# Kernel optimization log

Measured on AMD Instinct MI355X. Metric: run time of the kernel, lower is better.

## Reference

```python
import jax, jax.numpy as jnp
import numpy as np

B, N, E, IN, H, D = 4, 50000, 800000, 128, 4, 32
GAT_SLOPE = 0.2   # DGL GATConv leaky_relu negative_slope
ACT_SLOPE = 0.01  # nn.LeakyReLU default
BN_EPS = 1e-5


def _leaky(x, slope):
    return jnp.where(x >= 0, x, slope * x)


def setup_inputs() -> dict:
    key = jax.random.key(0)
    ks = jax.random.split(key, 6)
    xx = jax.random.normal(ks[0], (B, N, IN), dtype=jnp.float32)
    W = jax.random.normal(ks[1], (IN, H * D), dtype=jnp.float32) / np.sqrt(IN).astype(np.float32)
    attn_l = jax.random.normal(ks[2], (H, D), dtype=jnp.float32) * 0.1
    attn_r = jax.random.normal(ks[3], (H, D), dtype=jnp.float32) * 0.1
    gamma = jnp.ones((H * D,), dtype=jnp.float32)
    beta = jnp.zeros((H * D,), dtype=jnp.float32)
    src = jax.random.randint(ks[4], (E,), 0, N, dtype=jnp.int32)
    dst = jax.random.randint(ks[5], (E,), 0, N, dtype=jnp.int32)
    return {"xx": xx, "W": W, "attn_l": attn_l, "attn_r": attn_r,
            "gamma": gamma, "beta": beta, "src": src, "dst": dst}


def reference(xx, W, attn_l, attn_r, gamma, beta, src, dst):
    def gat_single(x):  # x: [N, IN]
        feat = (x @ W).reshape(N, H, D)                       # [N,H,D]
        el = jnp.einsum('nhd,hd->nh', feat, attn_l)           # [N,H]
        er = jnp.einsum('nhd,hd->nh', feat, attn_r)           # [N,H]
        e = _leaky(el[src] + er[dst], GAT_SLOPE)              # [E,H]
        # edge softmax over incoming edges of each dst node (stable)
        m = jax.ops.segment_max(e, dst, num_segments=N)       # [N,H]
        m = jnp.where(jnp.isfinite(m), m, 0.0)                # zero-in-degree guard
        w = jnp.exp(e - m[dst])                               # [E,H]
        denom = jax.ops.segment_sum(w, dst, num_segments=N)   # [N,H]
        alpha = w / jnp.maximum(denom[dst], 1e-9)             # [E,H]
        # scatter-weighted aggregation
        msg = alpha[:, :, None] * feat[src]                   # [E,H,D]
        return jax.ops.segment_sum(msg, dst, num_segments=N)  # [N,H,D]

    out = jax.vmap(gat_single)(xx)                            # [B,N,H,D]
    h = out.reshape(B, N, H * D)                              # flatten(2)
    # BatchNorm1d over channel dim (stats over B and N), training-mode batch stats
    mean = h.mean(axis=(0, 1))
    var = h.var(axis=(0, 1))
    hn = (h - mean) * jax.lax.rsqrt(var + BN_EPS) * gamma + beta
    return _leaky(hn, ACT_SLOPE)                              # [B,N,H*D]
```

## Files before the change

### kernel.cpp

```cpp
#include <hip/hip_runtime.h>
#include <math.h>

#define B_ 4
#define N_ 50000
#define E_ 800000
#define IN_ 128
#define H_ 4
#define D_ 32
#define HD_ 128
#define M_ (B_*N_)
#define GR_ 32

constexpr float GAT_SLOPE = 0.2f;
constexpr float ACT_SLOPE = 0.01f;
constexpr float BN_EPS = 1e-5f;

__device__ __forceinline__ unsigned short f2bf(float x) {
    unsigned u = __float_as_uint(x);
    unsigned r = (u + 0x7FFFu + ((u >> 16) & 1u)) >> 16;
    return (unsigned short)r;
}
__device__ __forceinline__ float bf2f(unsigned short h) {
    return __uint_as_float(((unsigned)h) << 16);
}

__global__ __launch_bounds__(256) void gemm_kernel(const float* __restrict__ xx,
                                                   const float* __restrict__ W,
                                                   const float* __restrict__ al,
                                                   const float* __restrict__ ar,
                                                   unsigned short* __restrict__ featb,
                                                   float* __restrict__ el,
                                                   float* __restrict__ er) {
    __shared__ float Ws[IN_ * HD_];
    __shared__ float Xs[GR_][IN_];
    const int tid = threadIdx.x;
    const long row0 = (long)blockIdx.x * GR_;

    for (int i = tid; i < IN_ * HD_ / 4; i += 256)
        ((float4*)Ws)[i] = ((const float4*)W)[i];
    for (int i = tid; i < GR_ * IN_ / 4; i += 256)
        ((float4*)Xs)[i] = ((const float4*)(xx + row0 * IN_))[i];
    __syncthreads();

    const int cl = tid & 31;
    const int r0 = (tid >> 5) * 4;
    float acc[4][4] = {};
#pragma unroll 4
    for (int k = 0; k < IN_; k += 4) {
        float4 w0 = *(const float4*)&Ws[(k + 0) * HD_ + 4 * cl];
        float4 w1 = *(const float4*)&Ws[(k + 1) * HD_ + 4 * cl];
        float4 w2 = *(const float4*)&Ws[(k + 2) * HD_ + 4 * cl];
        float4 w3 = *(const float4*)&Ws[(k + 3) * HD_ + 4 * cl];
#pragma unroll
        for (int i = 0; i < 4; ++i) {
            float4 xv = *(const float4*)&Xs[r0 + i][k];
            acc[i][0] = fmaf(xv.x, w0.x, acc[i][0]);
            acc[i][1] = fmaf(xv.x, w0.y, acc[i][1]);
            acc[i][2] = fmaf(xv.x, w0.z, acc[i][2]);
            acc[i][3] = fmaf(xv.x, w0.w, acc[i][3]);
            acc[i][0] = fmaf(xv.y, w1.x, acc[i][0]);
            acc[i][1] = fmaf(xv.y, w1.y, acc[i][1]);
            acc[i][2] = fmaf(xv.y, w1.z, acc[i][2]);
            acc[i][3] = fmaf(xv.y, w1.w, acc[i][3]);
            acc[i][0] = fmaf(xv.z, w2.x, acc[i][0]);
            acc[i][1] = fmaf(xv.z, w2.y, acc[i][1]);
            acc[i][2] = fmaf(xv.z, w2.z, acc[i][2]);
            acc[i][3] = fmaf(xv.z, w2.w, acc[i][3]);
            acc[i][0] = fmaf(xv.w, w3.x, acc[i][0]);
            acc[i][1] = fmaf(xv.w, w3.y, acc[i][1]);
            acc[i][2] = fmaf(xv.w, w3.z, acc[i][2]);
            acc[i][3] = fmaf(xv.w, w3.w, acc[i][3]);
        }
    }

    const float4 alv = *(const float4*)&al[4 * cl];
    const float4 arv = *(const float4*)&ar[4 * cl];
#pragma unroll
    for (int i = 0; i < 4; ++i) {
        long r = row0 + r0 + i;
        ushort4 pv;
        pv.x = f2bf(acc[i][0]); pv.y = f2bf(acc[i][1]);
        pv.z = f2bf(acc[i][2]); pv.w = f2bf(acc[i][3]);
        *(ushort4*)&featb[r * HD_ + 4 * cl] = pv;
        float pl = acc[i][0] * alv.x + acc[i][1] * alv.y + acc[i][2] * alv.z + acc[i][3] * alv.w;
        float pr = acc[i][0] * arv.x + acc[i][1] * arv.y + acc[i][2] * arv.z + acc[i][3] * arv.w;
#pragma unroll
        for (int o = 4; o; o >>= 1) {
            pl += __shfl_xor(pl, o, 64);
            pr += __shfl_xor(pr, o, 64);
        }
        if ((cl & 7) == 0) {
            int h = cl >> 3;
            el[r * H_ + h] = pl;
            er[r * H_ + h] = pr;
        }
    }
}

__global__ __launch_bounds__(256) void hist_kernel(const int* __restrict__ dst,
                                                   int* __restrict__ counts) {
    for (int e = blockIdx.x * 256 + threadIdx.x; e < E_; e += gridDim.x * 256)
        atomicAdd(&counts[dst[e]], 1);
}

__global__ __launch_bounds__(1024) void scan_kernel(const int* __restrict__ counts,
                                                    int* __restrict__ offsets,
                                                    int* __restrict__ cursor) {
    __shared__ int part[1024];
    const int tid = threadIdx.x;
    const int CH = (N_ + 1023) / 1024;
    const int base = tid * CH;
    int s = 0;
    for (int i = 0; i < CH; ++i) {
        int idx = base + i;
        if (idx < N_) s += counts[idx];
    }
    part[tid] = s;
    __syncthreads();
    for (int off = 1; off < 1024; off <<= 1) {
        int v = (tid >= off) ? part[tid - off] : 0;
        __syncthreads();
        part[tid] += v;
        __syncthreads();
    }
    int run = (tid == 0) ? 0 : part[tid - 1];
    for (int i = 0; i < CH; ++i) {
        int idx = base + i;
        if (idx < N_) {
            offsets[idx] = run;
            cursor[idx] = run;
            run += counts[idx];
        }
    }
    if (tid == 0) offsets[N_] = part[1023];
}

__global__ __launch_bounds__(256) void scatter_kernel(const int* __restrict__ src,
                                                      const int* __restrict__ dst,
                                                      int* __restrict__ cursor,
                                                      int* __restrict__ srcs) {
    for (int e = blockIdx.x * 256 + threadIdx.x; e < E_; e += gridDim.x * 256) {
        int pos = atomicAdd(&cursor[dst[e]], 1);
        srcs[pos] = src[e];
    }
}

__global__ __launch_bounds__(128) void aggregate_kernel(const int* __restrict__ offsets,
                                                        const int* __restrict__ srcs,
                                                        const float* __restrict__ el,
                                                        const float* __restrict__ er,
                                                        const unsigned short* __restrict__ featb,
                                                        float* __restrict__ out) {
    __shared__ int   s_idx[32];
    __shared__ float s_w[H_][32];
    const int t = threadIdx.x;
    const int h = t >> 5;
    const int lane = t & 31;
    const long bn = blockIdx.x;
    const int b = (int)(bn / N_);
    const int n = (int)(bn % N_);
    const long bbase = (long)b * N_;
    const int beg = offsets[n], end = offsets[n + 1];

    const float ern = er[(bbase + n) * H_ + h];
    const unsigned short* __restrict__ fb = featb + bbase * HD_ + t;

    float acc = 0.f, denom = 0.f;
    for (int c0 = beg; c0 < end; c0 += 32) {
        const int cnt = min(32, end - c0);
        int sj = 0;
        float w = 0.f;
        if (lane < cnt) {
            sj = srcs[c0 + lane];
            float ev = el[(bbase + sj) * H_ + h] + ern;
            ev = ev >= 0.f ? ev : GAT_SLOPE * ev;
            w = __expf(ev);
        }
        __syncthreads();
        s_w[h][lane] = w;
        if (h == 0) s_idx[lane] = sj;
        __syncthreads();
        denom += w;
        int j = 0;
        for (; j + 3 < cnt; j += 4) {
            int s0 = s_idx[j], s1 = s_idx[j + 1], s2 = s_idx[j + 2], s3 = s_idx[j + 3];
            float w0 = s_w[h][j], w1 = s_w[h][j + 1], w2 = s_w[h][j + 2], w3 = s_w[h][j + 3];
            float f0 = bf2f(fb[(long)s0 * HD_]);
            float f1 = bf2f(fb[(long)s1 * HD_]);
            float f2 = bf2f(fb[(long)s2 * HD_]);
            float f3 = bf2f(fb[(long)s3 * HD_]);
            acc = fmaf(w0, f0, acc);
            acc = fmaf(w1, f1, acc);
            acc = fmaf(w2, f2, acc);
            acc = fmaf(w3, f3, acc);
        }
        for (; j < cnt; ++j)
            acc = fmaf(s_w[h][j], bf2f(fb[(long)s_idx[j] * HD_]), acc);
    }
#pragma unroll
    for (int o = 16; o; o >>= 1) denom += __shfl_xor(denom, o, 32);
    out[bn * HD_ + t] = acc / fmaxf(denom, 1e-9f);
}

__global__ __launch_bounds__(256) void stats_kernel(const float* __restrict__ out,
                                                    float* __restrict__ chsum) {
    const int tid = threadIdx.x;
    const int c = tid & 127;
    const int half = tid >> 7;
    float s = 0.f, s2 = 0.f;
    for (long rp = blockIdx.x; rp < M_ / 2; rp += gridDim.x) {
        long row = rp * 2 + half;
        float v = out[row * HD_ + c];
        s += v;
        s2 += v * v;
    }
    __shared__ float red[512];
    red[tid] = s; red[256 + tid] = s2;
    __syncthreads();
    if (tid < 128) {
        s = red[tid] + red[tid + 128];
        s2 = red[256 + tid] + red[256 + tid + 128];
        atomicAdd(&chsum[c], s);
        atomicAdd(&chsum[128 + c], s2);
    }
}

__global__ void params_kernel(const float* __restrict__ chsum,
                              const float* __restrict__ gamma,
                              const float* __restrict__ beta,
                              float* __restrict__ ss) {
    int c = threadIdx.x;
    float mean = chsum[c] / (float)M_;
    float var = chsum[128 + c] / (float)M_ - mean * mean;
    float rstd = rsqrtf(var + BN_EPS);
    float sc = rstd * gamma[c];
    ss[c] = sc;
    ss[128 + c] = beta[c] - mean * sc;
}

__global__ __launch_bounds__(256) void norm_kernel(float* __restrict__ out,
                                                   const float* __restrict__ ss) {
    __shared__ float s_sc[128], s_sh[128];
    if (threadIdx.x < 128) {
        s_sc[threadIdx.x] = ss[threadIdx.x];
        s_sh[threadIdx.x] = ss[128 + threadIdx.x];
    }
    __syncthreads();
    const long total4 = (long)M_ * HD_ / 4;
    for (long i = (long)blockIdx.x * 256 + threadIdx.x; i < total4;
         i += (long)gridDim.x * 256) {
        float4 v = ((float4*)out)[i];
        int c = (int)((i & 31) << 2);
        float4 r;
        r.x = v.x * s_sc[c + 0] + s_sh[c + 0];
        r.y = v.y * s_sc[c + 1] + s_sh[c + 1];
        r.z = v.z * s_sc[c + 2] + s_sh[c + 2];
        r.w = v.w * s_sc[c + 3] + s_sh[c + 3];
        r.x = r.x >= 0.f ? r.x : ACT_SLOPE * r.x;
        r.y = r.y >= 0.f ? r.y : ACT_SLOPE * r.y;
        r.z = r.z >= 0.f ? r.z : ACT_SLOPE * r.z;
        r.w = r.w >= 0.f ? r.w : ACT_SLOPE * r.w;
        ((float4*)out)[i] = r;
    }
}

extern "C" void kernel_launch(void* const* d_in, const int* in_sizes, int n_in,
                              void* d_out, int out_size, void* d_ws, size_t ws_size,
                              hipStream_t stream) {
    const float* xx    = (const float*)d_in[0];
    const float* W     = (const float*)d_in[1];
    const float* al    = (const float*)d_in[2];
    const float* ar    = (const float*)d_in[3];
    const float* gamma = (const float*)d_in[4];
    const float* beta  = (const float*)d_in[5];
    const int*   src   = (const int*)d_in[6];
    const int*   dst   = (const int*)d_in[7];
    float* out = (float*)d_out;

    char* ws = (char*)d_ws;
    unsigned short* featb = (unsigned short*)ws; ws += (size_t)M_ * HD_ * 2;
    float* el      = (float*)ws;  ws += (size_t)M_ * H_ * 4;
    float* er      = (float*)ws;  ws += (size_t)M_ * H_ * 4;
    int*   counts  = (int*)ws;    ws += (size_t)N_ * 4;
    int*   offsets = (int*)ws;    ws += (size_t)(N_ + 1) * 4;
    int*   cursor  = (int*)ws;    ws += (size_t)N_ * 4;
    int*   srcs    = (int*)ws;    ws += (size_t)E_ * 4;
    float* chsum   = (float*)ws;  ws += 256 * 4;
    float* ss      = (float*)ws;  ws += 256 * 4;

    hipMemsetAsync(counts, 0, (size_t)N_ * 4, stream);
    hipMemsetAsync(chsum, 0, 256 * 4, stream);

    gemm_kernel<<<M_ / GR_, 256, 0, stream>>>(xx, W, al, ar, featb, el, er);
    hist_kernel<<<2048, 256, 0, stream>>>(dst, counts);
    scan_kernel<<<1, 1024, 0, stream>>>(counts, offsets, cursor);
    scatter_kernel<<<2048, 256, 0, stream>>>(src, dst, cursor, srcs);
    aggregate_kernel<<<M_, 128, 0, stream>>>(offsets, srcs, el, er, featb, out);
    stats_kernel<<<2048, 256, 0, stream>>>(out, chsum);
    params_kernel<<<1, 128, 0, stream>>>(chsum, gamma, beta, ss);
    norm_kernel<<<4096, 256, 0, stream>>>(out, ss);
}
```

Before: 814.6 us.

## Shrink aggregate to one wave with shuffles, XCD-aware mapping, persistent GEMM

The aggregate kernel now uses one 64-thread wave per destination node instead of a 128-thread block. Each lane handles two channels with 32-bit bf16-pair loads, and edge indices and weights are broadcast with shuffles rather than through shared memory and barriers. Blocks are remapped so that each group of 8 consecutive block IDs spans batch index and node parity, which appears intended to keep each batch's features on a fixed XCD's L2. The GEMM becomes persistent with 512 blocks so W is loaded into LDS once per block, not once per tile. The risks are a smaller edge chunk of 16 (more loop iterations) and less parallelism in the GEMM.

New measurement: 704.8 us. -13.5%, faster.

```diff
diff --git a/kernel.cpp b/kernel.cpp
--- a/kernel.cpp
+++ b/kernel.cpp
@@ -10,6 +10,7 @@
 #define HD_ 128
 #define M_ (B_*N_)
 #define GR_ 32
+#define GEMM_BLOCKS 512
 
 constexpr float GAT_SLOPE = 0.2f;
 constexpr float ACT_SLOPE = 0.01f;
@@ -20,8 +21,11 @@
     unsigned r = (u + 0x7FFFu + ((u >> 16) & 1u)) >> 16;
     return (unsigned short)r;
 }
-__device__ __forceinline__ float bf2f(unsigned short h) {
-    return __uint_as_float(((unsigned)h) << 16);
+__device__ __forceinline__ float bflo(unsigned u) {
+    return __uint_as_float(u << 16);
+}
+__device__ __forceinline__ float bfhi(unsigned u) {
+    return __uint_as_float(u & 0xFFFF0000u);
 }
 
 __global__ __launch_bounds__(256) void gemm_kernel(const float* __restrict__ xx,
@@ -34,65 +38,70 @@
     __shared__ float Ws[IN_ * HD_];
     __shared__ float Xs[GR_][IN_];
     const int tid = threadIdx.x;
-    const long row0 = (long)blockIdx.x * GR_;
+    const int cl = tid & 31;
+    const int r0 = (tid >> 5) * 4;
 
     for (int i = tid; i < IN_ * HD_ / 4; i += 256)
         ((float4*)Ws)[i] = ((const float4*)W)[i];
-    for (int i = tid; i < GR_ * IN_ / 4; i += 256)
-        ((float4*)Xs)[i] = ((const float4*)(xx + row0 * IN_))[i];
-    __syncthreads();
-
-    const int cl = tid & 31;
-    const int r0 = (tid >> 5) * 4;
-    float acc[4][4] = {};
+
+    const float4 alv = *(const float4*)&al[4 * cl];
+    const float4 arv = *(const float4*)&ar[4 * cl];
+
+    for (int tt = blockIdx.x; tt < M_ / GR_; tt += GEMM_BLOCKS) {
+        const long row0 = (long)tt * GR_;
+        __syncthreads();
+        for (int i = tid; i < GR_ * IN_ / 4; i += 256)
+            ((float4*)Xs)[i] = ((const float4*)(xx + row0 * IN_))[i];
+        __syncthreads();
+
+        float acc[4][4] = {};
 #pragma unroll 4
-    for (int k = 0; k < IN_; k += 4) {
-        float4 w0 = *(const float4*)&Ws[(k + 0) * HD_ + 4 * cl];
-        float4 w1 = *(const float4*)&Ws[(k + 1) * HD_ + 4 * cl];
-        float4 w2 = *(const float4*)&Ws[(k + 2) * HD_ + 4 * cl];
-        float4 w3 = *(const float4*)&Ws[(k + 3) * HD_ + 4 * cl];
+        for (int k = 0; k < IN_; k += 4) {
+            float4 w0 = *(const float4*)&Ws[(k + 0) * HD_ + 4 * cl];
+            float4 w1 = *(const float4*)&Ws[(k + 1) * HD_ + 4 * cl];
+            float4 w2 = *(const float4*)&Ws[(k + 2) * HD_ + 4 * cl];
+            float4 w3 = *(const float4*)&Ws[(k + 3) * HD_ + 4 * cl];
+#pragma unroll
+            for (int i = 0; i < 4; ++i) {
+                float4 xv = *(const float4*)&Xs[r0 + i][k];
+                acc[i][0] = fmaf(xv.x, w0.x, acc[i][0]);
+                acc[i][1] = fmaf(xv.x, w0.y, acc[i][1]);
+                acc[i][2] = fmaf(xv.x, w0.z, acc[i][2]);
+                acc[i][3] = fmaf(xv.x, w0.w, acc[i][3]);
+                acc[i][0] = fmaf(xv.y, w1.x, acc[i][0]);
+                acc[i][1] = fmaf(xv.y, w1.y, acc[i][1]);
+                acc[i][2] = fmaf(xv.y, w1.z, acc[i][2]);
+                acc[i][3] = fmaf(xv.y, w1.w, acc[i][3]);
+                acc[i][0] = fmaf(xv.z, w2.x, acc[i][0]);
+                acc[i][1] = fmaf(xv.z, w2.y, acc[i][1]);
+                acc[i][2] = fmaf(xv.z, w2.z, acc[i][2]);
+                acc[i][3] = fmaf(xv.z, w2.w, acc[i][3]);
+                acc[i][0] = fmaf(xv.w, w3.x, acc[i][0]);
+                acc[i][1] = fmaf(xv.w, w3.y, acc[i][1]);
+                acc[i][2] = fmaf(xv.w, w3.z, acc[i][2]);
+                acc[i][3] = fmaf(xv.w, w3.w, acc[i][3]);
+            }
+        }
+
 #pragma unroll
         for (int i = 0; i < 4; ++i) {
-            float4 xv = *(const float4*)&Xs[r0 + i][k];
-            acc[i][0] = fmaf(xv.x, w0.x, acc[i][0]);
-            acc[i][1] = fmaf(xv.x, w0.y, acc[i][1]);
-            acc[i][2] = fmaf(xv.x, w0.z, acc[i][2]);
-            acc[i][3] = fmaf(xv.x, w0.w, acc[i][3]);
-            acc[i][0] = fmaf(xv.y, w1.x, acc[i][0]);
-            acc[i][1] = fmaf(xv.y, w1.y, acc[i][1]);
-            acc[i][2] = fmaf(xv.y, w1.z, acc[i][2]);
-            acc[i][3] = fmaf(xv.y, w1.w, acc[i][3]);
-            acc[i][0] = fmaf(xv.z, w2.x, acc[i][0]);
-            acc[i][1] = fmaf(xv.z, w2.y, acc[i][1]);
-            acc[i][2] = fmaf(xv.z, w2.z, acc[i][2]);
-            acc[i][3] = fmaf(xv.z, w2.w, acc[i][3]);
-            acc[i][0] = fmaf(xv.w, w3.x, acc[i][0]);
-            acc[i][1] = fmaf(xv.w, w3.y, acc[i][1]);
-            acc[i][2] = fmaf(xv.w, w3.z, acc[i][2]);
-            acc[i][3] = fmaf(xv.w, w3.w, acc[i][3]);
-        }
-    }
-
-    const float4 alv = *(const float4*)&al[4 * cl];
-    const float4 arv = *(const float4*)&ar[4 * cl];
+            long r = row0 + r0 + i;
+            ushort4 pv;
+            pv.x = f2bf(acc[i][0]); pv.y = f2bf(acc[i][1]);
+            pv.z = f2bf(acc[i][2]); pv.w = f2bf(acc[i][3]);
+            *(ushort4*)&featb[r * HD_ + 4 * cl] = pv;
+            float pl = acc[i][0] * alv.x + acc[i][1] * alv.y + acc[i][2] * alv.z + acc[i][3] * alv.w;
+            float pr = acc[i][0] * arv.x + acc[i][1] * arv.y + acc[i][2] * arv.z + acc[i][3] * arv.w;
 #pragma unroll
-    for (int i = 0; i < 4; ++i) {
-        long r = row0 + r0 + i;
-        ushort4 pv;
-        pv.x = f2bf(acc[i][0]); pv.y = f2bf(acc[i][1]);
-        pv.z = f2bf(acc[i][2]); pv.w = f2bf(acc[i][3]);
-        *(ushort4*)&featb[r * HD_ + 4 * cl] = pv;
-        float pl = acc[i][0] * alv.x + acc[i][1] * alv.y + acc[i][2] * alv.z + acc[i][3] * alv.w;
-        float pr = acc[i][0] * arv.x + acc[i][1] * arv.y + acc[i][2] * arv.z + acc[i][3] * arv.w;
-#pragma unroll
-        for (int o = 4; o; o >>= 1) {
-            pl += __shfl_xor(pl, o, 64);
-            pr += __shfl_xor(pr, o, 64);
-        }
-        if ((cl & 7) == 0) {
-            int h = cl >> 3;
-            el[r * H_ + h] = pl;
-            er[r * H_ + h] = pr;
+            for (int o = 4; o; o >>= 1) {
+                pl += __shfl_xor(pl, o, 64);
+                pr += __shfl_xor(pr, o, 64);
+            }
+            if ((cl & 7) == 0) {
+                int h = cl >> 3;
+                el[r * H_ + h] = pl;
+                er[r * H_ + h] = pr;
+            }
         }
     }
 }
@@ -145,61 +154,72 @@
     }
 }
 
-__global__ __launch_bounds__(128) void aggregate_kernel(const int* __restrict__ offsets,
-                                                        const int* __restrict__ srcs,
-                                                        const float* __restrict__ el,
-                                                        const float* __restrict__ er,
-                                                        const unsigned short* __restrict__ featb,
-                                                        float* __restrict__ out) {
-    __shared__ int   s_idx[32];
-    __shared__ float s_w[H_][32];
+__global__ __launch_bounds__(64) void aggregate_kernel(const int* __restrict__ offsets,
+                                                       const int* __restrict__ srcs,
+                                                       const float* __restrict__ el,
+                                                       const float* __restrict__ er,
+                                                       const unsigned short* __restrict__ featb,
+                                                       float* __restrict__ out) {
     const int t = threadIdx.x;
-    const int h = t >> 5;
-    const int lane = t & 31;
-    const long bn = blockIdx.x;
-    const int b = (int)(bn / N_);
-    const int n = (int)(bn % N_);
+    const int h = t >> 4;
+    const int hb = t & 48;
+    const int t4 = 4 * t;
+    const unsigned g = blockIdx.x;
+    const int xcd = (int)(g & 7u);
+    const int b = xcd >> 1;
+    const int n = (int)((g >> 3) * 2 + (xcd & 1));
     const long bbase = (long)b * N_;
     const int beg = offsets[n], end = offsets[n + 1];
 
     const float ern = er[(bbase + n) * H_ + h];
-    const unsigned short* __restrict__ fb = featb + bbase * HD_ + t;
-
-    float acc = 0.f, denom = 0.f;
-    for (int c0 = beg; c0 < end; c0 += 32) {
-        const int cnt = min(32, end - c0);
-        int sj = 0;
+    const char* fbase = (const char*)(featb + bbase * HD_);
+    const int j16 = t & 15;
+
+    float acc0 = 0.f, acc1 = 0.f, dsum = 0.f;
+    for (int c0 = beg; c0 < end; c0 += 16) {
+        const int cnt = min(16, end - c0);
         float w = 0.f;
-        if (lane < cnt) {
-            sj = srcs[c0 + lane];
-            float ev = el[(bbase + sj) * H_ + h] + ern;
+        int off = 0;
+        if (j16 < cnt) {
+            int s = srcs[c0 + j16];
+            off = s << 8;
+            float ev = el[(bbase + s) * H_ + h] + ern;
             ev = ev >= 0.f ? ev : GAT_SLOPE * ev;
             w = __expf(ev);
         }
-        __syncthreads();
-        s_w[h][lane] = w;
-        if (h == 0) s_idx[lane] = sj;
-        __syncthreads();
-        denom += w;
+        dsum += w;
         int j = 0;
         for (; j + 3 < cnt; j += 4) {
-            int s0 = s_idx[j], s1 = s_idx[j + 1], s2 = s_idx[j + 2], s3 = s_idx[j + 3];
-            float w0 = s_w[h][j], w1 = s_w[h][j + 1], w2 = s_w[h][j + 2], w3 = s_w[h][j + 3];
-            float f0 = bf2f(fb[(long)s0 * HD_]);
-            float f1 = bf2f(fb[(long)s1 * HD_]);
-            float f2 = bf2f(fb[(long)s2 * HD_]);
-            float f3 = bf2f(fb[(long)s3 * HD_]);
-            acc = fmaf(w0, f0, acc);
-            acc = fmaf(w1, f1, acc);
-            acc = fmaf(w2, f2, acc);
-            acc = fmaf(w3, f3, acc);
-        }
-        for (; j < cnt; ++j)
-            acc = fmaf(s_w[h][j], bf2f(fb[(long)s_idx[j] * HD_]), acc);
+            int o0 = __shfl(off, j);
+            int o1 = __shfl(off, j + 1);
+            int o2 = __shfl(off, j + 2);
+            int o3 = __shfl(off, j + 3);
+            float w0 = __shfl(w, hb | j);
+            float w1 = __shfl(w, hb | (j + 1));
+            float w2 = __shfl(w, hb | (j + 2));
+            float w3 = __shfl(w, hb | (j + 3));
+            unsigned u0 = *(const unsigned*)(fbase + o0 + t4);
+            unsigned u1 = *(const unsigned*)(fbase + o1 + t4);
+            unsigned u2 = *(const unsigned*)(fbase + o2 + t4);
+            unsigned u3 = *(const unsigned*)(fbase + o3 + t4);
+            acc0 = fmaf(w0, bflo(u0), acc0); acc1 = fmaf(w0, bfhi(u0), acc1);
+            acc0 = fmaf(w1, bflo(u1), acc0); acc1 = fmaf(w1, bfhi(u1), acc1);
+            acc0 = fmaf(w2, bflo(u2), acc0); acc1 = fmaf(w2, bfhi(u2), acc1);
+            acc0 = fmaf(w3, bflo(u3), acc0); acc1 = fmaf(w3, bfhi(u3), acc1);
+        }
+        for (; j < cnt; ++j) {
+            int o0 = __shfl(off, j);
+            float w0 = __shfl(w, hb | j);
+            unsigned u0 = *(const unsigned*)(fbase + o0 + t4);
+            acc0 = fmaf(w0, bflo(u0), acc0);
+            acc1 = fmaf(w0, bfhi(u0), acc1);
+        }
     }
 #pragma unroll
-    for (int o = 16; o; o >>= 1) denom += __shfl_xor(denom, o, 32);
-    out[bn * HD_ + t] = acc / fmaxf(denom, 1e-9f);
+    for (int o = 8; o; o >>= 1) dsum += __shfl_xor(dsum, o, 64);
+    const float inv = 1.0f / fmaxf(dsum, 1e-9f);
+    float2 res = make_float2(acc0 * inv, acc1 * inv);
+    *(float2*)&out[((bbase + n) * HD_) + 2 * t] = res;
 }
 
 __global__ __launch_bounds__(256) void stats_kernel(const float* __restrict__ out,
@@ -291,11 +311,11 @@
     hipMemsetAsync(counts, 0, (size_t)N_ * 4, stream);
     hipMemsetAsync(chsum, 0, 256 * 4, stream);
 
-    gemm_kernel<<<M_ / GR_, 256, 0, stream>>>(xx, W, al, ar, featb, el, er);
+    gemm_kernel<<<GEMM_BLOCKS, 256, 0, stream>>>(xx, W, al, ar, featb, el, er);
     hist_kernel<<<2048, 256, 0, stream>>>(dst, counts);
     scan_kernel<<<1, 1024, 0, stream>>>(counts, offsets, cursor);
     scatter_kernel<<<2048, 256, 0, stream>>>(src, dst, cursor, srcs);
-    aggregate_kernel<<<M_, 128, 0, stream>>>(offsets, srcs, el, er, featb, out);
+    aggregate_kernel<<<M_, 64, 0, stream>>>(offsets, srcs, el, er, featb, out);
     stats_kernel<<<2048, 256, 0, stream>>>(out, chsum);
     params_kernel<<<1, 128, 0, stream>>>(chsum, gamma, beta, ss);
     norm_kernel<<<4096, 256, 0, stream>>>(out, ss);
```
